# Kernel optimization log

Measured on AMD Instinct MI355X. Metric: run time of the kernel, lower is better.

## Reference

```python
import jax, jax.numpy as jnp
import numpy as np
from jax import lax

VOCAB, EMB, RNN = 20000, 300, 512
B, NCLS, TWORDS = 64, 200, 8


def setup_inputs() -> dict:
    key = jax.random.key(0)
    ks = jax.random.split(key, 10)
    s = 0.05
    return {
        "sentence": jax.random.randint(ks[0], (B, NCLS, TWORDS), 0, VOCAB, dtype=jnp.int32),
        "word2vec": jax.random.normal(ks[1], (VOCAB, EMB), dtype=jnp.float32) * s,
        "W_ih1": jax.random.normal(ks[2], (4 * RNN, EMB), dtype=jnp.float32) * s,
        "W_hh1": jax.random.normal(ks[3], (4 * RNN, RNN), dtype=jnp.float32) * s,
        "b_ih1": jax.random.normal(ks[4], (4 * RNN,), dtype=jnp.float32) * s,
        "b_hh1": jax.random.normal(ks[5], (4 * RNN,), dtype=jnp.float32) * s,
        "W_ih2": jax.random.normal(ks[6], (4 * RNN, RNN), dtype=jnp.float32) * s,
        "W_hh2": jax.random.normal(ks[7], (4 * RNN, RNN), dtype=jnp.float32) * s,
        "b_ih2": jax.random.normal(ks[8], (4 * RNN,), dtype=jnp.float32) * s,
        "b_hh2": jax.random.normal(ks[9], (4 * RNN,), dtype=jnp.float32) * s,
    }


def _lstm_cell(x, h, c, W_ih, W_hh, b):
    # PyTorch LSTMCell gate order: i, f, g, o
    gates = x @ W_ih.T + h @ W_hh.T + b  # [BN, 4*RNN]
    i, f, g, o = jnp.split(gates, 4, axis=-1)
    c_new = jax.nn.sigmoid(f) * c + jax.nn.sigmoid(i) * jnp.tanh(g)
    h_new = jax.nn.sigmoid(o) * jnp.tanh(c_new)
    return h_new, c_new


def reference(sentence, word2vec, W_ih1, W_hh1, b_ih1, b_hh1, W_ih2, W_hh2, b_ih2, b_hh2):
    batch, num_class, max_words = sentence.shape
    bn = batch * num_class
    ids = sentence.reshape(bn, max_words)
    # embedding gather + tanh (dropout is identity in eval mode)
    emb = jnp.tanh(word2vec[ids])              # [BN, T, EMB]
    xs = jnp.swapaxes(emb, 0, 1)               # [T, BN, EMB]
    b1 = b_ih1 + b_hh1
    b2 = b_ih2 + b_hh2
    rnn = W_hh1.shape[1]
    zeros = jnp.zeros((bn, rnn), dtype=word2vec.dtype)
    init = (zeros, zeros, zeros, zeros)

    def step(carry, x):
        h1, c1, h2, c2 = carry
        h1, c1 = _lstm_cell(x, h1, c1, W_ih1, W_hh1, b1)
        h2, c2 = _lstm_cell(h1, h2, c2, W_ih2, W_hh2, b2)
        return (h1, c1, h2, c2), None

    (h1, c1, h2, c2), _ = lax.scan(step, init, xs)
    return h2.reshape(batch, num_class, rnn)
```

## Files before the change

### kernel.cpp

```cpp
#include <hip/hip_runtime.h>
#include <hip/hip_bf16.h>

#define BROWS  12800
#define TSTEPS 8
#define EMB    300
#define EMBP   320
#define RNN    512
#define NG     2048
#define K1     832
#define K2     1024

typedef short bf16x8 __attribute__((ext_vector_type(8)));
typedef float f32x4  __attribute__((ext_vector_type(4)));
typedef __hip_bfloat16 bf16;

__device__ __forceinline__ float sigmoidf_(float x) { return 1.f / (1.f + __expf(-x)); }
__device__ __forceinline__ float tanhf_(float x)    { return 1.f - 2.f / (__expf(2.f * x) + 1.f); }

__device__ __forceinline__ void gl_lds16(const bf16* g, bf16* l) {
    __builtin_amdgcn_global_load_lds(
        (const __attribute__((address_space(1))) void*)g,
        (__attribute__((address_space(3))) void*)l,
        16, 0, 0);
}

__global__ void convert_weights(const float* __restrict__ Wih1, const float* __restrict__ Whh1,
                                const float* __restrict__ Wih2, const float* __restrict__ Whh2,
                                const float* __restrict__ bih1, const float* __restrict__ bhh1,
                                const float* __restrict__ bih2, const float* __restrict__ bhh2,
                                bf16* __restrict__ Wc1, bf16* __restrict__ Wc2,
                                float* __restrict__ Bp1, float* __restrict__ Bp2) {
    int idx = blockIdx.x * 256 + threadIdx.x;
    const int n1 = NG * K1;
    const int n2 = NG * K2;
    if (idx < n1) {
        int n = idx / K1, k = idx - n * K1;
        int on = ((n >> 4) & 3) * RNN + (n >> 6) * 16 + (n & 15);
        float v = 0.f;
        if (k < EMB)        v = Wih1[on * EMB + k];
        else if (k >= EMBP) v = Whh1[on * RNN + (k - EMBP)];
        Wc1[idx] = __float2bfloat16(v);
    }
    if (idx < n2) {
        int n = idx >> 10, k = idx & (K2 - 1);
        int on = ((n >> 4) & 3) * RNN + (n >> 6) * 16 + (n & 15);
        float v = (k < RNN) ? Wih2[on * RNN + k] : Whh2[on * RNN + (k - RNN)];
        Wc2[idx] = __float2bfloat16(v);
    }
    if (idx < NG) {
        int on = ((idx >> 4) & 3) * RNN + (idx >> 6) * 16 + (idx & 15);
        Bp1[idx] = bih1[on] + bhh1[on];
        Bp2[idx] = bih2[on] + bhh2[on];
    }
}

__global__ void embed_step(const int* __restrict__ sent, const float* __restrict__ w2v,
                           bf16* __restrict__ Xbuf, int t) {
    int row = blockIdx.x;
    int col = threadIdx.x;
    int id  = sent[row * TSTEPS + t];
    float v = (col < EMB) ? tanhf_(w2v[id * EMB + col]) : 0.f;
    Xbuf[(size_t)row * EMBP + col] = __float2bfloat16(v);
}

#define BM 128
#define BN 128

__global__ __launch_bounds__(256, 4) void gemm_lstm(const bf16* __restrict__ Ax, int ldx, int ksplit,
                                                    const bf16* __restrict__ Ah, int ldh_in,
                                                    const bf16* __restrict__ W,
                                                    const float* __restrict__ Bp,
                                                    float* __restrict__ cst,
                                                    bf16* __restrict__ hdst, int ldh_out, int offh,
                                                    float* __restrict__ outf, int en_out,
                                                    int K) {
    __shared__ __attribute__((aligned(16))) bf16 sA[BM * 64];
    __shared__ __attribute__((aligned(16))) bf16 sB[BN * 64];

    const int tid  = threadIdx.x;
    const int lane = tid & 63;
    const int wave = tid >> 6;
    const int wm   = wave >> 1, wn = wave & 1;
    const int bn   = blockIdx.x;
    const int bm   = blockIdx.y;

    f32x4 acc[4][4];
#pragma unroll
    for (int i = 0; i < 4; ++i)
#pragma unroll
        for (int j = 0; j < 4; ++j)
#pragma unroll
            for (int r = 0; r < 4; ++r) acc[i][j][r] = 0.f;

    const int r = lane & 15, q = lane >> 4;

    int srow[4], scol[4];
#pragma unroll
    for (int c = 0; c < 4; ++c) {
        int ch = c * 256 + tid;
        srow[c] = ch >> 3;
        scol[c] = ((ch & 7) ^ (srow[c] & 7)) * 8;
    }
    const bf16* Wbase = W + (size_t)(bn * BN) * K;

    for (int kb = 0; kb < K; kb += 64) {
        const bf16* src; int ld, ko;
        if (kb < ksplit) { src = Ax; ld = ldx;    ko = kb; }
        else             { src = Ah; ld = ldh_in; ko = kb - ksplit; }
        src += (size_t)(bm * BM) * ld;
#pragma unroll
        for (int c = 0; c < 4; ++c) {
            int ch = c * 256 + tid;
            gl_lds16(src   + (size_t)srow[c] * ld + ko + scol[c], &sA[ch * 8]);
            gl_lds16(Wbase + (size_t)srow[c] * K  + kb + scol[c], &sB[ch * 8]);
        }
        __syncthreads();
#pragma unroll
        for (int kk = 0; kk < 64; kk += 32) {
            const int kc = kk >> 3;
            bf16x8 af[4], wf[4];
#pragma unroll
            for (int i = 0; i < 4; ++i)
                af[i] = *(const bf16x8*)(&sA[(wm * 64 + i * 16 + r) * 64 + (((q + kc) ^ (r & 7)) * 8)]);
#pragma unroll
            for (int j = 0; j < 4; ++j)
                wf[j] = *(const bf16x8*)(&sB[(wn * 64 + j * 16 + r) * 64 + (((q + kc) ^ (r & 7)) * 8)]);
#pragma unroll
            for (int i = 0; i < 4; ++i)
#pragma unroll
                for (int j = 0; j < 4; ++j)
                    acc[i][j] = __builtin_amdgcn_mfma_f32_16x16x32_bf16(
                        af[i], wf[j], acc[i][j], 0, 0, 0);
        }
        __syncthreads();
    }

    const int colb = bn * BN + wn * 64;
    const int u    = (2 * bn + wn) * 16 + r;
    const float bi = Bp[colb + r];
    const float bf = Bp[colb + 16 + r];
    const float bg = Bp[colb + 32 + r];
    const float bo = Bp[colb + 48 + r];

    float cc[4][4];
#pragma unroll
    for (int i = 0; i < 4; ++i)
#pragma unroll
        for (int rr = 0; rr < 4; ++rr) {
            int row = bm * BM + wm * 64 + i * 16 + q * 4 + rr;
            cc[i][rr] = cst[(size_t)row * RNN + u];
        }

#define HLD 40
#pragma unroll
    for (int i = 0; i < 4; ++i) {
#pragma unroll
        for (int rr = 0; rr < 4; ++rr) {
            int rowl = wm * 64 + i * 16 + q * 4 + rr;
            int row  = bm * BM + rowl;
            size_t cidx = (size_t)row * RNN + u;
            float gi = acc[i][0][rr] + bi;
            float gf = acc[i][1][rr] + bf;
            float gg = acc[i][2][rr] + bg;
            float go = acc[i][3][rr] + bo;
            float cn = sigmoidf_(gf) * cc[i][rr] + sigmoidf_(gi) * tanhf_(gg);
            float h  = sigmoidf_(go) * tanhf_(cn);
            cst[cidx] = cn;
            if (en_out) outf[cidx] = h;
            sA[rowl * HLD + wn * 16 + r] = __float2bfloat16(h);
        }
    }
    __syncthreads();

#pragma unroll
    for (int half = 0; half < 2; ++half) {
        int t    = half * 256 + tid;
        int rowl = t >> 2;
        int c8   = (t & 3) * 8;
        uint4 v  = *(const uint4*)&sA[rowl * HLD + c8];
        int row  = bm * BM + rowl;
        int gcol = bn * 32 + c8;
        *(uint4*)&hdst[(size_t)row * ldh_out + offh + gcol] = v;
    }
#undef HLD
}

extern "C" void kernel_launch(void* const* d_in, const int* in_sizes, int n_in,
                              void* d_out, int out_size, void* d_ws, size_t ws_size,
                              hipStream_t stream) {
    (void)in_sizes; (void)n_in; (void)out_size; (void)ws_size;
    const int*   sent = (const int*)d_in[0];
    const float* w2v  = (const float*)d_in[1];
    const float* Wih1 = (const float*)d_in[2];
    const float* Whh1 = (const float*)d_in[3];
    const float* bih1 = (const float*)d_in[4];
    const float* bhh1 = (const float*)d_in[5];
    const float* Wih2 = (const float*)d_in[6];
    const float* Whh2 = (const float*)d_in[7];
    const float* bih2 = (const float*)d_in[8];
    const float* bhh2 = (const float*)d_in[9];
    float* out = (float*)d_out;

    char* ws = (char*)d_ws;
    float* c1   = (float*)(ws);
    float* c2   = (float*)(ws + 26214400);
    bf16*  A2[2];
    A2[0] = (bf16*)(ws + 52428800);
    A2[1] = (bf16*)(ws + 78643200);
    bf16*  Xbuf = (bf16*) (ws + 104857600);
    bf16*  Wc1  = (bf16*) (ws + 113049600);
    bf16*  Wc2  = (bf16*) (ws + 116457472);
    float* Bp1  = (float*)(ws + 120651776);
    float* Bp2  = (float*)(ws + 120659968);

    hipMemsetAsync(ws, 0, 104857600, stream);

    convert_weights<<<dim3((NG * K2 + 255) / 256), dim3(256), 0, stream>>>(
        Wih1, Whh1, Wih2, Whh2, bih1, bhh1, bih2, bhh2, Wc1, Wc2, Bp1, Bp2);

    for (int t = 0; t < TSTEPS; ++t) {
        const int cur = t & 1, prv = cur ^ 1;

        embed_step<<<dim3(BROWS), dim3(EMBP), 0, stream>>>(sent, w2v, Xbuf, t);

        gemm_lstm<<<dim3(NG / BN, BROWS / BM), dim3(256), 0, stream>>>(
            Xbuf, EMBP, EMBP,
            A2[prv], K2,
            Wc1, Bp1, c1,
            A2[cur], K2, 0,
            (float*)nullptr, 0, K1);

        gemm_lstm<<<dim3(NG / BN, BROWS / BM), dim3(256), 0, stream>>>(
            (const bf16*)nullptr, 0, 0,
            A2[cur], K2,
            Wc2, Bp2, c2,
            A2[prv], K2, RNN,
            out, (t == TSTEPS - 1) ? 1 : 0, K2);
    }
}
```

Before: 1.207 ms.

## Use 256x256 double-buffered GEMM-LSTM tiles with interleaved MFMA and loads

The fused GEMM+LSTM kernel moves from 128x128 tiles with 256 threads to 256x256 tiles with 512 threads. It double-buffers LDS tiles through 128 KB of dynamic shared memory and interleaves the next tile's global-to-LDS loads with quarter-blocks of MFMA work, using explicit waitcnt, barriers and setprio. It also remaps block indices so consecutive blocks spread across XCDs. The aim is more reuse per loaded byte and hiding of memory latency behind matrix work. In exchange, the grid shrinks to 400 blocks, likely one per CU given the LDS size, which risks tail imbalance and lower occupancy.

```diff
diff --git a/kernel.cpp b/kernel.cpp
--- a/kernel.cpp
+++ b/kernel.cpp
@@ -63,123 +63,216 @@
     Xbuf[(size_t)row * EMBP + col] = __float2bfloat16(v);
 }
 
-#define BM 128
-#define BN 128
-
-__global__ __launch_bounds__(256, 4) void gemm_lstm(const bf16* __restrict__ Ax, int ldx, int ksplit,
-                                                    const bf16* __restrict__ Ah, int ldh_in,
-                                                    const bf16* __restrict__ W,
-                                                    const float* __restrict__ Bp,
-                                                    float* __restrict__ cst,
-                                                    bf16* __restrict__ hdst, int ldh_out, int offh,
-                                                    float* __restrict__ outf, int en_out,
-                                                    int K) {
-    __shared__ __attribute__((aligned(16))) bf16 sA[BM * 64];
-    __shared__ __attribute__((aligned(16))) bf16 sB[BN * 64];
+#define BM 256
+#define BN 256
+
+#define BAR()   __builtin_amdgcn_s_barrier()
+#define LGKM0() do { asm volatile("s_waitcnt lgkmcnt(0)" ::: "memory"); \
+                     __builtin_amdgcn_sched_barrier(0); } while (0)
+#define VMC(n)  do { asm volatile("s_waitcnt vmcnt(" #n ")" ::: "memory"); \
+                     __builtin_amdgcn_sched_barrier(0); } while (0)
+
+__global__ __launch_bounds__(512, 2) void gemm_lstm(
+        const bf16* __restrict__ Ax, int ldx, int ksplit,
+        const bf16* __restrict__ Ah, int ldh_in,
+        const bf16* __restrict__ W,
+        const float* __restrict__ Bp,
+        float* __restrict__ cst,
+        bf16* __restrict__ hdst, int ldh_out, int offh,
+        float* __restrict__ outf, int en_out,
+        int K) {
+    extern __shared__ __attribute__((aligned(16))) bf16 sh[];
 
     const int tid  = threadIdx.x;
     const int lane = tid & 63;
     const int wave = tid >> 6;
-    const int wm   = wave >> 1, wn = wave & 1;
-    const int bn   = blockIdx.x;
-    const int bm   = blockIdx.y;
-
-    f32x4 acc[4][4];
-#pragma unroll
-    for (int i = 0; i < 4; ++i)
+    const int wm   = wave >> 2, wn = wave & 3;
+
+    const int p0 = blockIdx.y * 8 + blockIdx.x;
+    const int lb = (p0 & 7) * 50 + (p0 >> 3);
+    const int bn = lb & 7;
+    const int bm = lb >> 3;
+
+    const int r = lane & 15, q = lane >> 4;
+    const int NT = K >> 6;
+
+    f32x4 acc[8][4];
+#pragma unroll
+    for (int i = 0; i < 8; ++i)
 #pragma unroll
         for (int j = 0; j < 4; ++j)
 #pragma unroll
-            for (int r = 0; r < 4; ++r) acc[i][j][r] = 0.f;
-
-    const int r = lane & 15, q = lane >> 4;
-
-    int srow[4], scol[4];
-#pragma unroll
-    for (int c = 0; c < 4; ++c) {
-        int ch = c * 256 + tid;
+            for (int rr = 0; rr < 4; ++rr) acc[i][j][rr] = 0.f;
+
+    int srow[2], scol[2];
+#pragma unroll
+    for (int c = 0; c < 2; ++c) {
+        int ch = c * 512 + tid;
         srow[c] = ch >> 3;
         scol[c] = ((ch & 7) ^ (srow[c] & 7)) * 8;
     }
-    const bf16* Wbase = W + (size_t)(bn * BN) * K;
-
-    for (int kb = 0; kb < K; kb += 64) {
+
+    auto stageA = [&](int tile) {
+        int kb = tile << 6;
         const bf16* src; int ld, ko;
         if (kb < ksplit) { src = Ax; ld = ldx;    ko = kb; }
         else             { src = Ah; ld = ldh_in; ko = kb - ksplit; }
         src += (size_t)(bm * BM) * ld;
-#pragma unroll
-        for (int c = 0; c < 4; ++c) {
-            int ch = c * 256 + tid;
-            gl_lds16(src   + (size_t)srow[c] * ld + ko + scol[c], &sA[ch * 8]);
-            gl_lds16(Wbase + (size_t)srow[c] * K  + kb + scol[c], &sB[ch * 8]);
-        }
-        __syncthreads();
-#pragma unroll
-        for (int kk = 0; kk < 64; kk += 32) {
-            const int kc = kk >> 3;
-            bf16x8 af[4], wf[4];
+        bf16* dst = sh + (tile & 1) * 32768;
+#pragma unroll
+        for (int h = 0; h < 2; ++h)
+#pragma unroll
+            for (int c = 0; c < 2; ++c) {
+                int ch = c * 512 + tid;
+                gl_lds16(src + (size_t)(h * 128 + srow[c]) * ld + ko + scol[c],
+                         dst + h * 8192 + ch * 8);
+            }
+    };
+    auto stageB = [&](int tile) {
+        int kb = tile << 6;
+        const bf16* src = W + (size_t)(bn * BN) * K;
+        bf16* dst = sh + (tile & 1) * 32768 + 16384;
+#pragma unroll
+        for (int h = 0; h < 2; ++h)
+#pragma unroll
+            for (int c = 0; c < 2; ++c) {
+                int ch = c * 512 + tid;
+                gl_lds16(src + (size_t)(h * 128 + srow[c]) * K + kb + scol[c],
+                         dst + h * 8192 + ch * 8);
+            }
+    };
+
+    stageA(0); stageB(0);
+    stageA(1); stageB(1);
+    VMC(8);
+    BAR();
+
+    bf16x8 af[8][2], bfr[4][2];
+    for (int t = 0; t < NT; ++t) {
+        const bf16* base = sh + (t & 1) * 32768;
+        const bf16* bA = base + wm * 8192;
+        const bf16* bB = base + 16384 + (wn >> 1) * 8192 + (wn & 1) * 4096;
+
+#pragma unroll
+        for (int i = 0; i < 4; ++i)
+#pragma unroll
+            for (int kk = 0; kk < 2; ++kk)
+                af[i][kk] = *(const bf16x8*)(bA + (i * 16 + r) * 64 + (((q + 4 * kk) ^ (r & 7)) * 8));
+#pragma unroll
+        for (int j = 0; j < 2; ++j)
+#pragma unroll
+            for (int kk = 0; kk < 2; ++kk)
+                bfr[j][kk] = *(const bf16x8*)(bB + (j * 16 + r) * 64 + (((q + 4 * kk) ^ (r & 7)) * 8));
+        __builtin_amdgcn_s_setprio(1);
+#pragma unroll
+        for (int kk = 0; kk < 2; ++kk)
 #pragma unroll
             for (int i = 0; i < 4; ++i)
-                af[i] = *(const bf16x8*)(&sA[(wm * 64 + i * 16 + r) * 64 + (((q + kc) ^ (r & 7)) * 8)]);
-#pragma unroll
-            for (int j = 0; j < 4; ++j)
-                wf[j] = *(const bf16x8*)(&sB[(wn * 64 + j * 16 + r) * 64 + (((q + kc) ^ (r & 7)) * 8)]);
+#pragma unroll
+                for (int j = 0; j < 2; ++j)
+                    acc[i][j] = __builtin_amdgcn_mfma_f32_16x16x32_bf16(
+                        af[i][kk], bfr[j][kk], acc[i][j], 0, 0, 0);
+        __builtin_amdgcn_s_setprio(0);
+        BAR();
+
+#pragma unroll
+        for (int i = 4; i < 8; ++i)
+#pragma unroll
+            for (int kk = 0; kk < 2; ++kk)
+                af[i][kk] = *(const bf16x8*)(bA + (i * 16 + r) * 64 + (((q + 4 * kk) ^ (r & 7)) * 8));
+        __builtin_amdgcn_s_setprio(1);
+#pragma unroll
+        for (int kk = 0; kk < 2; ++kk)
+#pragma unroll
+            for (int i = 4; i < 8; ++i)
+#pragma unroll
+                for (int j = 0; j < 2; ++j)
+                    acc[i][j] = __builtin_amdgcn_mfma_f32_16x16x32_bf16(
+                        af[i][kk], bfr[j][kk], acc[i][j], 0, 0, 0);
+        __builtin_amdgcn_s_setprio(0);
+        LGKM0();
+        BAR();
+
+        if (t + 2 < NT) stageA(t + 2);
+#pragma unroll
+        for (int j = 2; j < 4; ++j)
+#pragma unroll
+            for (int kk = 0; kk < 2; ++kk)
+                bfr[j][kk] = *(const bf16x8*)(bB + (j * 16 + r) * 64 + (((q + 4 * kk) ^ (r & 7)) * 8));
+        __builtin_amdgcn_s_setprio(1);
+#pragma unroll
+        for (int kk = 0; kk < 2; ++kk)
 #pragma unroll
             for (int i = 0; i < 4; ++i)
 #pragma unroll
-                for (int j = 0; j < 4; ++j)
+                for (int j = 2; j < 4; ++j)
                     acc[i][j] = __builtin_amdgcn_mfma_f32_16x16x32_bf16(
-                        af[i], wf[j], acc[i][j], 0, 0, 0);
-        }
-        __syncthreads();
-    }
+                        af[i][kk], bfr[j][kk], acc[i][j], 0, 0, 0);
+        __builtin_amdgcn_s_setprio(0);
+        LGKM0();
+        BAR();
+
+        if (t + 2 < NT) stageB(t + 2);
+        __builtin_amdgcn_s_setprio(1);
+#pragma unroll
+        for (int kk = 0; kk < 2; ++kk)
+#pragma unroll
+            for (int i = 4; i < 8; ++i)
+#pragma unroll
+                for (int j = 2; j < 4; ++j)
+                    acc[i][j] = __builtin_amdgcn_mfma_f32_16x16x32_bf16(
+                        af[i][kk], bfr[j][kk], acc[i][j], 0, 0, 0);
+        __builtin_amdgcn_s_setprio(0);
+        if (t + 2 < NT) { VMC(8); } else { VMC(0); }
+        BAR();
+    }
+    __syncthreads();
 
     const int colb = bn * BN + wn * 64;
-    const int u    = (2 * bn + wn) * 16 + r;
+    const int u    = (bn * 4 + wn) * 16 + r;
     const float bi = Bp[colb + r];
-    const float bf = Bp[colb + 16 + r];
+    const float bff = Bp[colb + 16 + r];
     const float bg = Bp[colb + 32 + r];
     const float bo = Bp[colb + 48 + r];
 
-    float cc[4][4];
-#pragma unroll
-    for (int i = 0; i < 4; ++i)
+    float cc[8][4];
+#pragma unroll
+    for (int i = 0; i < 8; ++i)
 #pragma unroll
         for (int rr = 0; rr < 4; ++rr) {
-            int row = bm * BM + wm * 64 + i * 16 + q * 4 + rr;
+            int row = bm * BM + wm * 128 + i * 16 + q * 4 + rr;
             cc[i][rr] = cst[(size_t)row * RNN + u];
         }
 
-#define HLD 40
-#pragma unroll
-    for (int i = 0; i < 4; ++i) {
+#define HLD 72
+#pragma unroll
+    for (int i = 0; i < 8; ++i) {
 #pragma unroll
         for (int rr = 0; rr < 4; ++rr) {
-            int rowl = wm * 64 + i * 16 + q * 4 + rr;
+            int rowl = wm * 128 + i * 16 + q * 4 + rr;
             int row  = bm * BM + rowl;
             size_t cidx = (size_t)row * RNN + u;
             float gi = acc[i][0][rr] + bi;
-            float gf = acc[i][1][rr] + bf;
+            float gf = acc[i][1][rr] + bff;
             float gg = acc[i][2][rr] + bg;
             float go = acc[i][3][rr] + bo;
             float cn = sigmoidf_(gf) * cc[i][rr] + sigmoidf_(gi) * tanhf_(gg);
             float h  = sigmoidf_(go) * tanhf_(cn);
             cst[cidx] = cn;
             if (en_out) outf[cidx] = h;
-            sA[rowl * HLD + wn * 16 + r] = __float2bfloat16(h);
+            sh[rowl * HLD + wn * 16 + r] = __float2bfloat16(h);
         }
     }
     __syncthreads();
 
 #pragma unroll
-    for (int half = 0; half < 2; ++half) {
-        int t    = half * 256 + tid;
-        int rowl = t >> 2;
-        int c8   = (t & 3) * 8;
-        uint4 v  = *(const uint4*)&sA[rowl * HLD + c8];
+    for (int hh = 0; hh < 4; ++hh) {
+        int t2   = hh * 512 + tid;
+        int rowl = t2 >> 3;
+        int c8   = (t2 & 7) * 8;
+        uint4 v  = *(const uint4*)&sh[rowl * HLD + c8];
         int row  = bm * BM + rowl;
-        int gcol = bn * 32 + c8;
+        int gcol = bn * 64 + c8;
         *(uint4*)&hdst[(size_t)row * ldh_out + offh + gcol] = v;
     }
 #undef HLD
@@ -213,6 +306,13 @@
     float* Bp1  = (float*)(ws + 120651776);
     float* Bp2  = (float*)(ws + 120659968);
 
+    static int shmem_set = 0;
+    if (!shmem_set) {
+        (void)hipFuncSetAttribute((const void*)gemm_lstm,
+                                  hipFuncAttributeMaxDynamicSharedMemorySize, 131072);
+        shmem_set = 1;
+    }
+
     hipMemsetAsync(ws, 0, 104857600, stream);
 
     convert_weights<<<dim3((NG * K2 + 255) / 256), dim3(256), 0, stream>>>(
@@ -223,14 +323,14 @@
 
         embed_step<<<dim3(BROWS), dim3(EMBP), 0, stream>>>(sent, w2v, Xbuf, t);
 
-        gemm_lstm<<<dim3(NG / BN, BROWS / BM), dim3(256), 0, stream>>>(
+        gemm_lstm<<<dim3(NG / BN, BROWS / BM), dim3(512), 131072, stream>>>(
             Xbuf, EMBP, EMBP,
             A2[prv], K2,
             Wc1, Bp1, c1,
             A2[cur], K2, 0,
             (float*)nullptr, 0, K1);
 
-        gemm_lstm<<<dim3(NG / BN, BROWS / BM), dim3(256), 0, stream>>>(
+        gemm_lstm<<<dim3(NG / BN, BROWS / BM), dim3(512), 131072, stream>>>(
             (const bf16*)nullptr, 0, 0,
             A2[cur], K2,
             Wc2, Bp2, c2,
```

After: 1.414 ms. 1.17x slower.
